# Kernel tuning notes

Measured on AMD Instinct MI355X. Metric: run time of the kernel, lower is better.

The kernel has to match this reference:

```python
import jax, jax.numpy as jnp
import numpy as np

EPS = 1e-6

def _rms(x, w):
    # RMSNorm over last dim with learned scale w
    var = jnp.mean(x * x, axis=-1, keepdims=True)
    return x * jax.lax.rsqrt(var + EPS) * w

def _split_heads(x, h):
    b, l, hd = x.shape
    return x.reshape(b, l, h, hd // h).transpose(0, 2, 1, 3)  # b h l d

def setup_inputs() -> dict:
    key = jax.random.key(0)
    ks = jax.random.split(key, 12)
    D = 2048          # hidden_size == ip_hidden_states_dim
    H = 16            # n_heads
    Dh = 128          # head_dim
    T = 1280          # timesteps_emb_dim
    B, L, Lip = 2, 2048, 512
    s = 0.02
    return {
        "ip_hidden_states": jax.random.normal(ks[0], (B, Lip, D), jnp.float32),
        "img_query": jax.random.normal(ks[1], (B, L, D), jnp.float32),
        "img_key": jax.random.normal(ks[2], (B, L, D), jnp.float32),
        "img_value": jax.random.normal(ks[3], (B, L, D), jnp.float32),
        "t_emb": jax.random.normal(ks[4], (B, T), jnp.float32),
        "W_ada": jax.random.normal(ks[5], (2 * D, T), jnp.float32) * s,
        "b_ada": jax.random.normal(ks[6], (2 * D,), jnp.float32) * s,
        "W_k_ip": jax.random.normal(ks[7], (D, D), jnp.float32) * s,
        "W_v_ip": jax.random.normal(ks[8], (D, D), jnp.float32) * s,
        "w_q": jnp.ones((Dh,), jnp.float32),
        "w_k": jnp.ones((Dh,), jnp.float32),
        "w_ipk": jnp.ones((Dh,), jnp.float32),
        "n_heads": H,
    }

def reference(ip_hidden_states, img_query, img_key, img_value, t_emb,
              W_ada, b_ada, W_k_ip, W_v_ip, w_q, w_k, w_ipk, n_heads):
    D = img_query.shape[-1]
    # AdaLayerNorm (mode='normal'): silu -> linear -> shift/scale, LN(no affine)
    emb = jax.nn.silu(t_emb) @ W_ada.T + b_ada          # [B, 2D]
    shift, scale = emb[:, :D], emb[:, D:]
    x = ip_hidden_states
    mu = jnp.mean(x, axis=-1, keepdims=True)
    var = jnp.mean((x - mu) ** 2, axis=-1, keepdims=True)
    xn = (x - mu) * jax.lax.rsqrt(var + 1e-6)
    ip_n = xn * (1.0 + scale[:, None, :]) + shift[:, None, :]
    # K/V projections for IP tokens
    ip_key = ip_n @ W_k_ip.T
    ip_value = ip_n @ W_v_ip.T
    # split heads
    q = _split_heads(img_query, n_heads)   # b h L d
    k = _split_heads(img_key, n_heads)
    v = _split_heads(img_value, n_heads)
    kip = _split_heads(ip_key, n_heads)    # b h Lip d
    vip = _split_heads(ip_value, n_heads)
    # RMSNorms
    q = _rms(q, w_q)
    k = _rms(k, w_k)
    kip = _rms(kip, w_ipk)
    # concat image + IP along sequence
    kcat = jnp.concatenate([k, kip], axis=2)
    vcat = jnp.concatenate([v, vip], axis=2)
    # SDPA
    d = q.shape[-1]
    scores = jnp.einsum('bhld,bhmd->bhlm', q, kcat) / jnp.sqrt(jnp.asarray(d, q.dtype))
    attn = jax.nn.softmax(scores, axis=-1)
    out = jnp.einsum('bhlm,bhmd->bhld', attn, vcat)
    b, h, l, dh = out.shape
    return out.transpose(0, 2, 1, 3).reshape(b, l, h * dh)
```

## Files before the change

### kernel.cpp

```cpp
#include <hip/hip_runtime.h>
#include <hip/hip_bf16.h>

typedef __attribute__((ext_vector_type(8))) __bf16 bf16x8;
typedef __attribute__((ext_vector_type(2))) __bf16 bf16x2;
typedef __attribute__((ext_vector_type(4))) float floatx4;
typedef __attribute__((ext_vector_type(2))) unsigned int uint2v;

#define DEV static __device__ __forceinline__

typedef __attribute__((address_space(1))) const unsigned int gu32;
typedef __attribute__((address_space(3))) unsigned int lu32;

DEV void dma16(const void* g, void* l) {
  __builtin_amdgcn_global_load_lds((gu32*)g, (lu32*)l, 16, 0, 0);
}

DEV unsigned short f2bf(float f) {
  unsigned int u = __float_as_uint(f);
  u += 0x7fffu + ((u >> 16) & 1u);
  return (unsigned short)(u >> 16);
}

DEV unsigned int pk_bf16(float a, float b) {
#if __has_builtin(__builtin_amdgcn_cvt_pk_bf16_f32)
  bf16x2 r = __builtin_amdgcn_cvt_pk_bf16_f32(a, b);
  union { bf16x2 v; unsigned int u; } c; c.v = r;
  return c.u;
#else
  return (unsigned int)f2bf(a) | ((unsigned int)f2bf(b) << 16);
#endif
}

DEV float wred_sum(float v) {
#pragma unroll
  for (int o = 32; o > 0; o >>= 1) v += __shfl_xor(v, o, 64);
  return v;
}

DEV floatx4 mfma32(bf16x8 a, bf16x8 b, floatx4 c) {
  return __builtin_amdgcn_mfma_f32_16x16x32_bf16(a, b, c, 0, 0, 0);
}

#if __has_builtin(__builtin_amdgcn_permlane32_swap) && __has_builtin(__builtin_amdgcn_permlane16_swap)
#define HAS_PLSWAP 1
DEV void p32sw(unsigned int& a, unsigned int& b) {
  uint2v r = __builtin_amdgcn_permlane32_swap(a, b, false, false);
  a = r[0]; b = r[1];
}
DEV void p16sw(unsigned int& a, unsigned int& b) {
  uint2v r = __builtin_amdgcn_permlane16_swap(a, b, false, false);
  a = r[0]; b = r[1];
}
#endif

__global__ void ada_kernel(const float* __restrict__ t_emb, const float* __restrict__ W_ada,
                           const float* __restrict__ b_ada, float* __restrict__ emb) {
  int w = threadIdx.x >> 6, lane = threadIdx.x & 63;
  int gid = blockIdx.x * 4 + w;
  int b = gid >> 12, n = gid & 4095;
  const float* te = t_emb + (size_t)b * 1280;
  const float* wr = W_ada + (size_t)n * 1280;
  float acc = 0.f;
#pragma unroll
  for (int i = 0; i < 20; ++i) {
    int t = lane + i * 64;
    float x = te[t];
    float s = x / (1.f + __expf(-x));
    acc += s * wr[t];
  }
  acc = wred_sum(acc);
  if (lane == 0) emb[gid] = acc + b_ada[n];
}

__global__ void ln_mod_kernel(const float* __restrict__ ip, const float* __restrict__ emb,
                              unsigned short* __restrict__ ipn) {
  int row = blockIdx.x;
  int b = row >> 9;
  int tid = threadIdx.x;
  const float* x = ip + (size_t)row * 2048;
  float xv[8];
  float s1 = 0.f, s2 = 0.f;
  {
    float4 x0 = *(const float4*)&x[tid * 8];
    float4 x1 = *(const float4*)&x[tid * 8 + 4];
    xv[0] = x0.x; xv[1] = x0.y; xv[2] = x0.z; xv[3] = x0.w;
    xv[4] = x1.x; xv[5] = x1.y; xv[6] = x1.z; xv[7] = x1.w;
#pragma unroll
    for (int i = 0; i < 8; ++i) { s1 += xv[i]; s2 += xv[i] * xv[i]; }
  }
  s1 = wred_sum(s1); s2 = wred_sum(s2);
  __shared__ float r1[4], r2[4];
  int w = tid >> 6, lane = tid & 63;
  if (lane == 0) { r1[w] = s1; r2[w] = s2; }
  __syncthreads();
  s1 = r1[0] + r1[1] + r1[2] + r1[3];
  s2 = r2[0] + r2[1] + r2[2] + r2[3];
  float mu = s1 * (1.f / 2048.f);
  float var = s2 * (1.f / 2048.f) - mu * mu;
  float rs = rsqrtf(var + 1e-6f);
  const float* sh = emb + (size_t)b * 4096;
  unsigned short* y = ipn + (size_t)row * 2048;
  unsigned short ob[8];
#pragma unroll
  for (int i = 0; i < 8; ++i) {
    int d = tid * 8 + i;
    float v = (xv[i] - mu) * rs;
    v = v * (1.f + sh[2048 + d]) + sh[d];
    ob[i] = f2bf(v);
  }
  int dst = (tid & ~7) | ((tid & 7) ^ (row & 7));
  *(uint4*)&y[dst * 8] = *(const uint4*)ob;
}

__global__ void cvtw_kernel(const float* __restrict__ wk, const float* __restrict__ wv,
                            unsigned short* __restrict__ wk16, unsigned short* __restrict__ wv16) {
  int row = blockIdx.x, tid = threadIdx.x;
  size_t gi = (size_t)row * 2048 + tid * 8;
  int dst = (tid & ~7) | ((tid & 7) ^ (row & 7));
  size_t o = (size_t)row * 2048 + (size_t)dst * 8;
  float4 a0 = *(const float4*)(wk + gi), a1 = *(const float4*)(wk + gi + 4);
  float4 b0 = *(const float4*)(wv + gi), b1 = *(const float4*)(wv + gi + 4);
  unsigned short oa[8] = { f2bf(a0.x), f2bf(a0.y), f2bf(a0.z), f2bf(a0.w),
                           f2bf(a1.x), f2bf(a1.y), f2bf(a1.z), f2bf(a1.w) };
  unsigned short ob[8] = { f2bf(b0.x), f2bf(b0.y), f2bf(b0.z), f2bf(b0.w),
                           f2bf(b1.x), f2bf(b1.y), f2bf(b1.z), f2bf(b1.w) };
  *(uint4*)(wk16 + o) = *(const uint4*)oa;
  *(uint4*)(wv16 + o) = *(const uint4*)ob;
}

__global__ __launch_bounds__(256) void proj_gemm(const unsigned short* __restrict__ A,
    const unsigned short* __restrict__ Wk, const unsigned short* __restrict__ Wv,
    float* __restrict__ Ck, float* __restrict__ Cv) {
  const unsigned short* Bm = blockIdx.z ? Wv : Wk;
  float* C = blockIdx.z ? Cv : Ck;
  int n0 = blockIdx.x * 64, m0 = blockIdx.y * 128;
  __shared__ __align__(16) unsigned char smem[49152];
  int tid = threadIdx.x, w = tid >> 6, lane = tid & 63, quad = lane >> 4, l16 = lane & 15;
  int xr = l16 & 7;
  floatx4 acc[2][4];
#pragma unroll
  for (int i = 0; i < 2; ++i)
#pragma unroll
    for (int j = 0; j < 4; ++j) { floatx4 z = {0.f, 0.f, 0.f, 0.f}; acc[i][j] = z; }

  const char* Abase = (const char*)A + (size_t)m0 * 4096;
  const char* Bbase = (const char*)Bm + (size_t)n0 * 4096;
  auto stage = [&](int buf, int kk) {
    char* As = (char*)(smem + buf * 24576);
    char* Bs = (char*)(smem + buf * 24576 + 16384);
#pragma unroll
    for (int j = 0; j < 4; ++j) {
      int idx = (w * 4 + j) * 64 + lane;
      dma16(Abase + (size_t)(idx >> 3) * 4096 + kk * 2 + (idx & 7) * 16,
            As + (w * 4 + j) * 1024);
    }
#pragma unroll
    for (int j = 0; j < 2; ++j) {
      int idx = (w * 2 + j) * 64 + lane;
      dma16(Bbase + (size_t)(idx >> 3) * 4096 + kk * 2 + (idx & 7) * 16,
            Bs + (w * 2 + j) * 1024);
    }
  };

  stage(0, 0);
  __syncthreads();
  for (int t = 0; t < 32; ++t) {
    int cur = t & 1;
    if (t < 31) stage(cur ^ 1, (t + 1) * 64);
    const unsigned short* As = (const unsigned short*)(smem + cur * 24576);
    const unsigned short* Bs = (const unsigned short*)(smem + cur * 24576 + 16384);
#pragma unroll
    for (int cc = 0; cc < 2; ++cc) {
      int pc = ((quad + 4 * cc) ^ xr) * 8;
      bf16x8 a0 = *(const bf16x8*)&As[(w * 32 + l16) * 64 + pc];
      bf16x8 a1 = *(const bf16x8*)&As[(w * 32 + 16 + l16) * 64 + pc];
#pragma unroll
      for (int nt = 0; nt < 4; ++nt) {
        bf16x8 bb = *(const bf16x8*)&Bs[(nt * 16 + l16) * 64 + pc];
        acc[0][nt] = mfma32(a0, bb, acc[0][nt]);
        acc[1][nt] = mfma32(a1, bb, acc[1][nt]);
      }
    }
    __syncthreads();
  }
#pragma unroll
  for (int rt = 0; rt < 2; ++rt)
#pragma unroll
    for (int nt = 0; nt < 4; ++nt)
#pragma unroll
      for (int r = 0; r < 4; ++r)
        C[(size_t)(m0 + w * 32 + rt * 16 + quad * 4 + r) * 2048 + n0 + nt * 16 + l16] = acc[rt][nt][r];
}

struct us4 { unsigned short a, b, c, d; };
__global__ __launch_bounds__(256) void kv_build(const float* __restrict__ img_key, const float* __restrict__ img_value,
                         const float* __restrict__ ipk, const float* __restrict__ ipv,
                         const float* __restrict__ w_k, const float* __restrict__ w_ipk,
                         unsigned short* __restrict__ Kc, unsigned short* __restrict__ VtT) {
  int bh = blockIdx.x;
  int mt = blockIdx.y;
  int b = bh >> 4, hh = bh & 15;
  int m0 = mt * 64;
  __shared__ __align__(16) unsigned short Vs[64 * 132];
  int tid = threadIdx.x;
  int mrow = tid >> 2, dq = tid & 3;
  int m = m0 + mrow;
  size_t base;
  const float* wsrc;
  const float *ksrc, *vsrc;
  if (m < 2048) {
    base = (size_t)(b * 2048 + m) * 2048 + hh * 128;
    ksrc = img_key + base; vsrc = img_value + base; wsrc = w_k;
  } else {
    base = (size_t)(b * 512 + (m - 2048)) * 2048 + hh * 128;
    ksrc = ipk + base; vsrc = ipv + base; wsrc = w_ipk;
  }
  float kvv[32]; float ss = 0.f;
  const float4* k4 = (const float4*)ksrc;
#pragma unroll
  for (int i = 0; i < 8; ++i) {
    float4 x = k4[dq * 8 + i];
    kvv[i * 4 + 0] = x.x; kvv[i * 4 + 1] = x.y; kvv[i * 4 + 2] = x.z; kvv[i * 4 + 3] = x.w;
    ss += x.x * x.x + x.y * x.y + x.z * x.z + x.w * x.w;
  }
  ss += __shfl_xor(ss, 1, 64);
  ss += __shfl_xor(ss, 2, 64);
  float rs = rsqrtf(ss * (1.f / 128.f) + 1e-6f);
  unsigned short kb[32];
#pragma unroll
  for (int j = 0; j < 32; ++j) kb[j] = f2bf(kvv[j] * rs * wsrc[dq * 32 + j]);
  uint4* kdst = (uint4*)&Kc[((size_t)bh * 2560 + m) * 128];
#pragma unroll
  for (int i = 0; i < 4; ++i) kdst[(dq * 4 + i) ^ (m & 7)] = ((const uint4*)kb)[i];
  const float4* v4 = (const float4*)vsrc;
#pragma unroll
  for (int i = 0; i < 8; ++i) {
    float4 x = v4[dq * 8 + i];
    us4 p = { f2bf(x.x), f2bf(x.y), f2bf(x.z), f2bf(x.w) };
    *(us4*)&Vs[mrow * 132 + dq * 32 + i * 4] = p;
  }
  __syncthreads();
  int d = tid >> 1, half = tid & 1;
  unsigned short ob[32];
#pragma unroll
  for (int j = 0; j < 32; ++j) ob[j] = Vs[(half * 32 + j) * 132 + d];
  uint4* vdst = (uint4*)&VtT[((size_t)(bh * 40 + mt)) * 8192 + d * 64];
#pragma unroll
  for (int i = 0; i < 4; ++i) vdst[(half * 4 + i) ^ (d & 7)] = ((const uint4*)ob)[i];
}

__global__ __launch_bounds__(256, 2) void attn_kernel(const float* __restrict__ Qf,
    const float* __restrict__ w_q,
    const unsigned short* __restrict__ Kc, const unsigned short* __restrict__ VtT,
    float* __restrict__ out) {
  const float SCL = 0.12751744f;
  const float FM = 17.0f;
  int n = blockIdx.x;
  int xcd = n & 7, jj = n >> 3;
  int bh = xcd * 4 + (jj >> 4);
  int qt2 = jj & 15;
  int b = bh >> 4, hh = bh & 15;
  int tid = threadIdx.x, w = tid >> 6, lane = tid & 63, quad = lane >> 4, l16 = lane & 15;
  int xr = l16 & 7;

  __shared__ __align__(16) unsigned char smem[65536];

  int q0 = qt2 * 128;

  bf16x8 aq[2][4];
#pragma unroll
  for (int qtl = 0; qtl < 2; ++qtl) {
    int qrow = q0 + w * 32 + qtl * 16 + l16;
    const float* src = Qf + ((size_t)(b * 2048 + qrow)) * 2048 + hh * 128;
    float xs[32]; float ss = 0.f;
#pragma unroll
    for (int c = 0; c < 4; ++c) {
      float4 a = *(const float4*)&src[quad * 8 + c * 32];
      float4 b2 = *(const float4*)&src[quad * 8 + c * 32 + 4];
      xs[c * 8 + 0] = a.x;  xs[c * 8 + 1] = a.y;  xs[c * 8 + 2] = a.z;  xs[c * 8 + 3] = a.w;
      xs[c * 8 + 4] = b2.x; xs[c * 8 + 5] = b2.y; xs[c * 8 + 6] = b2.z; xs[c * 8 + 7] = b2.w;
      ss += a.x * a.x + a.y * a.y + a.z * a.z + a.w * a.w
          + b2.x * b2.x + b2.y * b2.y + b2.z * b2.z + b2.w * b2.w;
    }
    ss += __shfl_xor(ss, 16, 64);
    ss += __shfl_xor(ss, 32, 64);
    float rs = rsqrtf(ss * (1.f / 128.f) + 1e-6f);
#pragma unroll
    for (int c = 0; c < 4; ++c) {
      float4 wa = *(const float4*)&w_q[quad * 8 + c * 32];
      float4 wb = *(const float4*)&w_q[quad * 8 + c * 32 + 4];
      union { unsigned int u[4]; bf16x8 v; } pk;
      pk.u[0] = pk_bf16(xs[c * 8 + 0] * rs * wa.x, xs[c * 8 + 1] * rs * wa.y);
      pk.u[1] = pk_bf16(xs[c * 8 + 2] * rs * wa.z, xs[c * 8 + 3] * rs * wa.w);
      pk.u[2] = pk_bf16(xs[c * 8 + 4] * rs * wb.x, xs[c * 8 + 5] * rs * wb.y);
      pk.u[3] = pk_bf16(xs[c * 8 + 6] * rs * wb.z, xs[c * 8 + 7] * rs * wb.w);
      aq[qtl][c] = pk.v;
    }
  }

  const unsigned short* Kb = Kc + (size_t)bh * 2560 * 128;
  const unsigned short* Vb = VtT + (size_t)bh * 40 * 8192;

  floatx4 acc[2][8];
#pragma unroll
  for (int i = 0; i < 2; ++i)
#pragma unroll
    for (int j = 0; j < 8; ++j) { floatx4 z = {0.f, 0.f, 0.f, 0.f}; acc[i][j] = z; }
  float rsum[2] = {0.f, 0.f};

  int seg = w * 4;
  auto stage = [&](int buf, int t) {
    const unsigned short* Ksrc = Kb + (size_t)t * 8192;
    const unsigned short* Vsrc = Vb + (size_t)t * 8192;
    unsigned short* Kt = (unsigned short*)(smem + buf * 32768);
    unsigned short* Vd = (unsigned short*)(smem + buf * 32768 + 16384);
#pragma unroll
    for (int j = 0; j < 4; ++j) {
      int off = (seg + j) * 512 + lane * 8;
      dma16(Ksrc + off, Kt + (seg + j) * 512);
      dma16(Vsrc + off, Vd + (seg + j) * 512);
    }
  };

  stage(0, 0);
  __syncthreads();

  for (int t = 0; t < 40; ++t) {
    int cur = t & 1;
    if (t < 39) stage(cur ^ 1, t + 1);
    const unsigned short* Kt = (const unsigned short*)(smem + cur * 32768);
    const unsigned short* Vs = (const unsigned short*)(smem + cur * 32768 + 16384);

    floatx4 sacc[4][2];
#pragma unroll
    for (int ms = 0; ms < 4; ++ms)
#pragma unroll
      for (int j = 0; j < 2; ++j) { floatx4 z = {0.f, 0.f, 0.f, 0.f}; sacc[ms][j] = z; }
#pragma unroll
    for (int ms = 0; ms < 4; ++ms) {
      int krow = (ms * 16 + l16) * 128;
#pragma unroll
      for (int c = 0; c < 4; ++c) {
        bf16x8 bk = *(const bf16x8*)&Kt[krow + ((quad + c * 4) ^ xr) * 8];
        sacc[ms][0] = mfma32(bk, aq[0][c], sacc[ms][0]);
        sacc[ms][1] = mfma32(bk, aq[1][c], sacc[ms][1]);
      }
    }

    union { unsigned int u[4]; bf16x8 v; } pf[2][2];
#pragma unroll
    for (int mc = 0; mc < 2; ++mc) {
#pragma unroll
      for (int qtl = 0; qtl < 2; ++qtl) {
        float pA[4], pB[4];
#pragma unroll
        for (int r = 0; r < 4; ++r) {
          pA[r] = __builtin_amdgcn_exp2f(fmaf(sacc[mc * 2][qtl][r], SCL, -FM));
          pB[r] = __builtin_amdgcn_exp2f(fmaf(sacc[mc * 2 + 1][qtl][r], SCL, -FM));
        }
        rsum[qtl] += (pA[0] + pA[1]) + (pA[2] + pA[3])
                   + (pB[0] + pB[1]) + (pB[2] + pB[3]);
        unsigned int R0 = pk_bf16(pA[0], pA[1]);
        unsigned int R1 = pk_bf16(pA[2], pA[3]);
        unsigned int R2 = pk_bf16(pB[0], pB[1]);
        unsigned int R3 = pk_bf16(pB[2], pB[3]);
#ifdef HAS_PLSWAP
        p32sw(R0, R2);
        p32sw(R1, R3);
        p16sw(R0, R2);
        p16sw(R1, R3);
        pf[mc][qtl].u[0] = R0; pf[mc][qtl].u[1] = R1;
        pf[mc][qtl].u[2] = R2; pf[mc][qtl].u[3] = R3;
#else
        int base = ((quad & 1) * 2) * 16 + l16;
        int base2 = base + 16;
        unsigned int a0 = __shfl((int)R0, base, 64),  b0 = __shfl((int)R2, base, 64);
        unsigned int a1 = __shfl((int)R1, base, 64),  b1 = __shfl((int)R3, base, 64);
        unsigned int a2 = __shfl((int)R0, base2, 64), b2 = __shfl((int)R2, base2, 64);
        unsigned int a3 = __shfl((int)R1, base2, 64), b3 = __shfl((int)R3, base2, 64);
        bool hi = (quad >> 1) != 0;
        pf[mc][qtl].u[0] = hi ? b0 : a0;
        pf[mc][qtl].u[1] = hi ? b1 : a1;
        pf[mc][qtl].u[2] = hi ? b2 : a2;
        pf[mc][qtl].u[3] = hi ? b3 : a3;
#endif
      }
    }

#pragma unroll
    for (int dt = 0; dt < 8; ++dt) {
      int vrow = (dt * 16 + l16) * 64;
#pragma unroll
      for (int mc = 0; mc < 2; ++mc) {
        bf16x8 va = *(const bf16x8*)&Vs[vrow + ((mc * 4 + quad) ^ xr) * 8];
        acc[0][dt] = mfma32(va, pf[mc][0].v, acc[0][dt]);
        acc[1][dt] = mfma32(va, pf[mc][1].v, acc[1][dt]);
      }
    }
    __syncthreads();
  }

  rsum[0] += __shfl_xor(rsum[0], 16, 64); rsum[0] += __shfl_xor(rsum[0], 32, 64);
  rsum[1] += __shfl_xor(rsum[1], 16, 64); rsum[1] += __shfl_xor(rsum[1], 32, 64);
#pragma unroll
  for (int qtl = 0; qtl < 2; ++qtl) {
    float inv = 1.f / rsum[qtl];
    int qrow = q0 + w * 32 + qtl * 16 + l16;
    float* orow = out + ((size_t)(b * 2048 + qrow)) * 2048 + hh * 128;
#pragma unroll
    for (int dt = 0; dt < 8; ++dt) {
      floatx4 r = acc[qtl][dt] * inv;
      *(floatx4*)&orow[dt * 16 + quad * 4] = r;
    }
  }
}

extern "C" void kernel_launch(void* const* d_in, const int* in_sizes, int n_in,
                              void* d_out, int out_size, void* d_ws, size_t ws_size,
                              hipStream_t stream) {
  const float* ip    = (const float*)d_in[0];
  const float* q     = (const float*)d_in[1];
  const float* k     = (const float*)d_in[2];
  const float* v     = (const float*)d_in[3];
  const float* temb  = (const float*)d_in[4];
  const float* wada  = (const float*)d_in[5];
  const float* bada  = (const float*)d_in[6];
  const float* wkip  = (const float*)d_in[7];
  const float* wvip  = (const float*)d_in[8];
  const float* w_q   = (const float*)d_in[9];
  const float* w_k   = (const float*)d_in[10];
  const float* w_ipk = (const float*)d_in[11];
  float* out = (float*)d_out;
  char* ws = (char*)d_ws;

  float* emb           = (float*)(ws + 0);
  unsigned short* ipn  = (unsigned short*)(ws + 32768);
  unsigned short* wk16 = (unsigned short*)(ws + 4227072);
  unsigned short* wv16 = (unsigned short*)(ws + 12615680);
  unsigned short* Kcat = (unsigned short*)(ws + 16777216);
  unsigned short* VtT  = (unsigned short*)(ws + 37748736);
  float* ipk           = (float*)(ws + 58720256);
  float* ipv           = (float*)(ws + 67108864);

  ada_kernel<<<dim3(2048), dim3(256), 0, stream>>>(temb, wada, bada, emb);
  ln_mod_kernel<<<dim3(1024), dim3(256), 0, stream>>>(ip, emb, ipn);
  cvtw_kernel<<<dim3(2048), dim3(256), 0, stream>>>(wkip, wvip, wk16, wv16);
  proj_gemm<<<dim3(32, 8, 2), dim3(256), 0, stream>>>(ipn, wk16, wv16, ipk, ipv);
  kv_build<<<dim3(32, 40), dim3(256), 0, stream>>>(k, v, ipk, ipv, w_k, w_ipk, Kcat, VtT);
  attn_kernel<<<dim3(512), dim3(256), 0, stream>>>(q, w_q, Kcat, VtT, out);
}
```

Before: 330.6 us.

## Merge LN and weight-convert kernels, enlarge GEMM and attention tiles to 512 threads

Fuses the LayerNorm-modulate and weight bf16 conversion into one launch that branches on block index. The projection GEMM moves to 128x128 tiles with 512 threads and an XCD-aware block mapping, and attention processes 256 query rows per 512-thread block so each K/V tile staged in LDS is shared by twice as many rows. The aim is fewer launches, more reuse of staged K/V and GEMM operand tiles, and less global traffic. The cost is fewer blocks in flight, which can hurt latency hiding, plus higher register pressure now that the attention kernel no longer requests 2 blocks per CU.

```diff
diff --git a/kernel.cpp b/kernel.cpp
--- a/kernel.cpp
+++ b/kernel.cpp
@@ -72,92 +72,97 @@
   if (lane == 0) emb[gid] = acc + b_ada[n];
 }
 
-__global__ void ln_mod_kernel(const float* __restrict__ ip, const float* __restrict__ emb,
-                              unsigned short* __restrict__ ipn) {
-  int row = blockIdx.x;
-  int b = row >> 9;
+__global__ void lncvt_kernel(const float* __restrict__ ip, const float* __restrict__ emb,
+                             unsigned short* __restrict__ ipn,
+                             const float* __restrict__ wk, const float* __restrict__ wv,
+                             unsigned short* __restrict__ wk16, unsigned short* __restrict__ wv16) {
+  int blk = blockIdx.x;
   int tid = threadIdx.x;
-  const float* x = ip + (size_t)row * 2048;
-  float xv[8];
-  float s1 = 0.f, s2 = 0.f;
-  {
-    float4 x0 = *(const float4*)&x[tid * 8];
-    float4 x1 = *(const float4*)&x[tid * 8 + 4];
-    xv[0] = x0.x; xv[1] = x0.y; xv[2] = x0.z; xv[3] = x0.w;
-    xv[4] = x1.x; xv[5] = x1.y; xv[6] = x1.z; xv[7] = x1.w;
-#pragma unroll
-    for (int i = 0; i < 8; ++i) { s1 += xv[i]; s2 += xv[i] * xv[i]; }
-  }
-  s1 = wred_sum(s1); s2 = wred_sum(s2);
-  __shared__ float r1[4], r2[4];
-  int w = tid >> 6, lane = tid & 63;
-  if (lane == 0) { r1[w] = s1; r2[w] = s2; }
-  __syncthreads();
-  s1 = r1[0] + r1[1] + r1[2] + r1[3];
-  s2 = r2[0] + r2[1] + r2[2] + r2[3];
-  float mu = s1 * (1.f / 2048.f);
-  float var = s2 * (1.f / 2048.f) - mu * mu;
-  float rs = rsqrtf(var + 1e-6f);
-  const float* sh = emb + (size_t)b * 4096;
-  unsigned short* y = ipn + (size_t)row * 2048;
-  unsigned short ob[8];
-#pragma unroll
-  for (int i = 0; i < 8; ++i) {
-    int d = tid * 8 + i;
-    float v = (xv[i] - mu) * rs;
-    v = v * (1.f + sh[2048 + d]) + sh[d];
-    ob[i] = f2bf(v);
-  }
-  int dst = (tid & ~7) | ((tid & 7) ^ (row & 7));
-  *(uint4*)&y[dst * 8] = *(const uint4*)ob;
-}
-
-__global__ void cvtw_kernel(const float* __restrict__ wk, const float* __restrict__ wv,
-                            unsigned short* __restrict__ wk16, unsigned short* __restrict__ wv16) {
-  int row = blockIdx.x, tid = threadIdx.x;
-  size_t gi = (size_t)row * 2048 + tid * 8;
-  int dst = (tid & ~7) | ((tid & 7) ^ (row & 7));
-  size_t o = (size_t)row * 2048 + (size_t)dst * 8;
-  float4 a0 = *(const float4*)(wk + gi), a1 = *(const float4*)(wk + gi + 4);
-  float4 b0 = *(const float4*)(wv + gi), b1 = *(const float4*)(wv + gi + 4);
-  unsigned short oa[8] = { f2bf(a0.x), f2bf(a0.y), f2bf(a0.z), f2bf(a0.w),
-                           f2bf(a1.x), f2bf(a1.y), f2bf(a1.z), f2bf(a1.w) };
-  unsigned short ob[8] = { f2bf(b0.x), f2bf(b0.y), f2bf(b0.z), f2bf(b0.w),
-                           f2bf(b1.x), f2bf(b1.y), f2bf(b1.z), f2bf(b1.w) };
-  *(uint4*)(wk16 + o) = *(const uint4*)oa;
-  *(uint4*)(wv16 + o) = *(const uint4*)ob;
-}
-
-__global__ __launch_bounds__(256) void proj_gemm(const unsigned short* __restrict__ A,
+  if (blk < 1024) {
+    int row = blk;
+    int b = row >> 9;
+    const float* x = ip + (size_t)row * 2048;
+    float xv[8];
+    float s1 = 0.f, s2 = 0.f;
+    {
+      float4 x0 = *(const float4*)&x[tid * 8];
+      float4 x1 = *(const float4*)&x[tid * 8 + 4];
+      xv[0] = x0.x; xv[1] = x0.y; xv[2] = x0.z; xv[3] = x0.w;
+      xv[4] = x1.x; xv[5] = x1.y; xv[6] = x1.z; xv[7] = x1.w;
+#pragma unroll
+      for (int i = 0; i < 8; ++i) { s1 += xv[i]; s2 += xv[i] * xv[i]; }
+    }
+    s1 = wred_sum(s1); s2 = wred_sum(s2);
+    __shared__ float r1[4], r2[4];
+    int w = tid >> 6, lane = tid & 63;
+    if (lane == 0) { r1[w] = s1; r2[w] = s2; }
+    __syncthreads();
+    s1 = r1[0] + r1[1] + r1[2] + r1[3];
+    s2 = r2[0] + r2[1] + r2[2] + r2[3];
+    float mu = s1 * (1.f / 2048.f);
+    float var = s2 * (1.f / 2048.f) - mu * mu;
+    float rs = rsqrtf(var + 1e-6f);
+    const float* sh = emb + (size_t)b * 4096;
+    unsigned short* y = ipn + (size_t)row * 2048;
+    unsigned short ob[8];
+#pragma unroll
+    for (int i = 0; i < 8; ++i) {
+      int d = tid * 8 + i;
+      float v = (xv[i] - mu) * rs;
+      v = v * (1.f + sh[2048 + d]) + sh[d];
+      ob[i] = f2bf(v);
+    }
+    int dst = (tid & ~7) | ((tid & 7) ^ (row & 7));
+    *(uint4*)&y[dst * 8] = *(const uint4*)ob;
+  } else {
+    int row = blk - 1024;
+    size_t gi = (size_t)row * 2048 + tid * 8;
+    int dst = (tid & ~7) | ((tid & 7) ^ (row & 7));
+    size_t o = (size_t)row * 2048 + (size_t)dst * 8;
+    float4 a0 = *(const float4*)(wk + gi), a1 = *(const float4*)(wk + gi + 4);
+    float4 b0 = *(const float4*)(wv + gi), b1 = *(const float4*)(wv + gi + 4);
+    unsigned short oa[8] = { f2bf(a0.x), f2bf(a0.y), f2bf(a0.z), f2bf(a0.w),
+                             f2bf(a1.x), f2bf(a1.y), f2bf(a1.z), f2bf(a1.w) };
+    unsigned short ob2[8] = { f2bf(b0.x), f2bf(b0.y), f2bf(b0.z), f2bf(b0.w),
+                              f2bf(b1.x), f2bf(b1.y), f2bf(b1.z), f2bf(b1.w) };
+    *(uint4*)(wk16 + o) = *(const uint4*)oa;
+    *(uint4*)(wv16 + o) = *(const uint4*)ob2;
+  }
+}
+
+__global__ __launch_bounds__(512) void proj_gemm(const unsigned short* __restrict__ A,
     const unsigned short* __restrict__ Wk, const unsigned short* __restrict__ Wv,
     float* __restrict__ Ck, float* __restrict__ Cv) {
-  const unsigned short* Bm = blockIdx.z ? Wv : Wk;
-  float* C = blockIdx.z ? Cv : Ck;
-  int n0 = blockIdx.x * 64, m0 = blockIdx.y * 128;
-  __shared__ __align__(16) unsigned char smem[49152];
+  int n = blockIdx.x;
+  int xcd = n & 7, idx = n >> 3;
+  int by = idx & 7;
+  int bxl = idx >> 3;
+  int z = xcd >> 2;
+  int bx = (xcd & 3) * 4 + bxl;
+  const unsigned short* Bm = z ? Wv : Wk;
+  float* C = z ? Cv : Ck;
+  int n0 = bx * 128, m0 = by * 128;
+  __shared__ __align__(16) unsigned char smem[65536];
   int tid = threadIdx.x, w = tid >> 6, lane = tid & 63, quad = lane >> 4, l16 = lane & 15;
   int xr = l16 & 7;
+  int wm = w >> 1, wn = w & 1;
   floatx4 acc[2][4];
 #pragma unroll
   for (int i = 0; i < 2; ++i)
 #pragma unroll
-    for (int j = 0; j < 4; ++j) { floatx4 z = {0.f, 0.f, 0.f, 0.f}; acc[i][j] = z; }
+    for (int j = 0; j < 4; ++j) { floatx4 z2 = {0.f, 0.f, 0.f, 0.f}; acc[i][j] = z2; }
 
   const char* Abase = (const char*)A + (size_t)m0 * 4096;
   const char* Bbase = (const char*)Bm + (size_t)n0 * 4096;
   auto stage = [&](int buf, int kk) {
-    char* As = (char*)(smem + buf * 24576);
-    char* Bs = (char*)(smem + buf * 24576 + 16384);
-#pragma unroll
-    for (int j = 0; j < 4; ++j) {
-      int idx = (w * 4 + j) * 64 + lane;
-      dma16(Abase + (size_t)(idx >> 3) * 4096 + kk * 2 + (idx & 7) * 16,
-            As + (w * 4 + j) * 1024);
-    }
+    char* As = (char*)(smem + buf * 32768);
+    char* Bs = (char*)(smem + buf * 32768 + 16384);
 #pragma unroll
     for (int j = 0; j < 2; ++j) {
-      int idx = (w * 2 + j) * 64 + lane;
-      dma16(Bbase + (size_t)(idx >> 3) * 4096 + kk * 2 + (idx & 7) * 16,
+      int idx2 = (w * 2 + j) * 64 + lane;
+      dma16(Abase + (size_t)(idx2 >> 3) * 4096 + kk * 2 + (idx2 & 7) * 16,
+            As + (w * 2 + j) * 1024);
+      dma16(Bbase + (size_t)(idx2 >> 3) * 4096 + kk * 2 + (idx2 & 7) * 16,
             Bs + (w * 2 + j) * 1024);
     }
   };
@@ -167,16 +172,16 @@
   for (int t = 0; t < 32; ++t) {
     int cur = t & 1;
     if (t < 31) stage(cur ^ 1, (t + 1) * 64);
-    const unsigned short* As = (const unsigned short*)(smem + cur * 24576);
-    const unsigned short* Bs = (const unsigned short*)(smem + cur * 24576 + 16384);
+    const unsigned short* As = (const unsigned short*)(smem + cur * 32768);
+    const unsigned short* Bs = (const unsigned short*)(smem + cur * 32768 + 16384);
 #pragma unroll
     for (int cc = 0; cc < 2; ++cc) {
       int pc = ((quad + 4 * cc) ^ xr) * 8;
-      bf16x8 a0 = *(const bf16x8*)&As[(w * 32 + l16) * 64 + pc];
-      bf16x8 a1 = *(const bf16x8*)&As[(w * 32 + 16 + l16) * 64 + pc];
+      bf16x8 a0 = *(const bf16x8*)&As[(wm * 32 + l16) * 64 + pc];
+      bf16x8 a1 = *(const bf16x8*)&As[(wm * 32 + 16 + l16) * 64 + pc];
 #pragma unroll
       for (int nt = 0; nt < 4; ++nt) {
-        bf16x8 bb = *(const bf16x8*)&Bs[(nt * 16 + l16) * 64 + pc];
+        bf16x8 bb = *(const bf16x8*)&Bs[(wn * 64 + nt * 16 + l16) * 64 + pc];
         acc[0][nt] = mfma32(a0, bb, acc[0][nt]);
         acc[1][nt] = mfma32(a1, bb, acc[1][nt]);
       }
@@ -189,7 +194,7 @@
     for (int nt = 0; nt < 4; ++nt)
 #pragma unroll
       for (int r = 0; r < 4; ++r)
-        C[(size_t)(m0 + w * 32 + rt * 16 + quad * 4 + r) * 2048 + n0 + nt * 16 + l16] = acc[rt][nt][r];
+        C[(size_t)(m0 + wm * 32 + rt * 16 + quad * 4 + r) * 2048 + n0 + wn * 64 + nt * 16 + l16] = acc[rt][nt][r];
 }
 
 struct us4 { unsigned short a, b, c, d; };
@@ -249,7 +254,7 @@
   for (int i = 0; i < 4; ++i) vdst[(half * 4 + i) ^ (d & 7)] = ((const uint4*)ob)[i];
 }
 
-__global__ __launch_bounds__(256, 2) void attn_kernel(const float* __restrict__ Qf,
+__global__ __launch_bounds__(512) void attn_kernel(const float* __restrict__ Qf,
     const float* __restrict__ w_q,
     const unsigned short* __restrict__ Kc, const unsigned short* __restrict__ VtT,
     float* __restrict__ out) {
@@ -257,15 +262,15 @@
   const float FM = 17.0f;
   int n = blockIdx.x;
   int xcd = n & 7, jj = n >> 3;
-  int bh = xcd * 4 + (jj >> 4);
-  int qt2 = jj & 15;
+  int bh = xcd * 4 + (jj >> 3);
+  int qt3 = jj & 7;
   int b = bh >> 4, hh = bh & 15;
   int tid = threadIdx.x, w = tid >> 6, lane = tid & 63, quad = lane >> 4, l16 = lane & 15;
   int xr = l16 & 7;
 
   __shared__ __align__(16) unsigned char smem[65536];
 
-  int q0 = qt2 * 128;
+  int q0 = qt3 * 256;
 
   bf16x8 aq[2][4];
 #pragma unroll
@@ -308,14 +313,14 @@
     for (int j = 0; j < 8; ++j) { floatx4 z = {0.f, 0.f, 0.f, 0.f}; acc[i][j] = z; }
   float rsum[2] = {0.f, 0.f};
 
-  int seg = w * 4;
+  int seg = w * 2;
   auto stage = [&](int buf, int t) {
     const unsigned short* Ksrc = Kb + (size_t)t * 8192;
     const unsigned short* Vsrc = Vb + (size_t)t * 8192;
     unsigned short* Kt = (unsigned short*)(smem + buf * 32768);
     unsigned short* Vd = (unsigned short*)(smem + buf * 32768 + 16384);
 #pragma unroll
-    for (int j = 0; j < 4; ++j) {
+    for (int j = 0; j < 2; ++j) {
       int off = (seg + j) * 512 + lane * 8;
       dma16(Ksrc + off, Kt + (seg + j) * 512);
       dma16(Vsrc + off, Vd + (seg + j) * 512);
@@ -443,9 +448,8 @@
   float* ipv           = (float*)(ws + 67108864);
 
   ada_kernel<<<dim3(2048), dim3(256), 0, stream>>>(temb, wada, bada, emb);
-  ln_mod_kernel<<<dim3(1024), dim3(256), 0, stream>>>(ip, emb, ipn);
-  cvtw_kernel<<<dim3(2048), dim3(256), 0, stream>>>(wkip, wvip, wk16, wv16);
-  proj_gemm<<<dim3(32, 8, 2), dim3(256), 0, stream>>>(ipn, wk16, wv16, ipk, ipv);
+  lncvt_kernel<<<dim3(3072), dim3(256), 0, stream>>>(ip, emb, ipn, wkip, wvip, wk16, wv16);
+  proj_gemm<<<dim3(256), dim3(512), 0, stream>>>(ipn, wk16, wv16, ipk, ipv);
   kv_build<<<dim3(32, 40), dim3(256), 0, stream>>>(k, v, ipk, ipv, w_k, w_ipk, Kcat, VtT);
-  attn_kernel<<<dim3(512), dim3(256), 0, stream>>>(q, w_q, Kcat, VtT, out);
-}
+  attn_kernel<<<dim3(256), dim3(512), 0, stream>>>(q, w_q, Kcat, VtT, out);
+}
```

After: 341.3 us. 3.2% more time.
